# Performance work log

Measured on AMD Instinct MI355X. Metric: run time of the kernel, lower is better.

The kernel has to match this reference:

```python
import jax, jax.numpy as jnp
import numpy as np

NUM_EXPERTS = 8
TOP_K = 2
N_EMBD = 1024
D_FFN = 2048  # 4*N_EMBD // TOP_K, already multiple of BLOCK_N=128
BLOCK_M = 128
NORM_TOPK = True


def setup_inputs() -> dict:
    key = jax.random.key(0)
    k1, k2, k3 = jax.random.split(key, 3)
    x = jax.random.normal(k1, (2, 2048, N_EMBD), dtype=jnp.float32)
    router_w = jax.random.normal(k2, (NUM_EXPERTS, N_EMBD), dtype=jnp.float32) * 0.02
    w1 = jax.random.normal(k3, (N_EMBD, D_FFN * NUM_EXPERTS), dtype=jnp.float32) * 0.02
    return {"x": x, "router_w": router_w, "w1": w1}


def reference(x, router_w, w1):
    B, S, H = x.shape
    x_flat = x.reshape(-1, H)                                   # [T, H]
    router_logits = x_flat @ router_w.T                         # [T, E]
    probs = jax.nn.softmax(router_logits.astype(jnp.float32), axis=-1)
    rweights, sel = jax.lax.top_k(probs, TOP_K)                 # [T, k]
    if NORM_TOPK:
        rweights = rweights / rweights.sum(axis=-1, keepdims=True)
    rweights = rweights.astype(x.dtype)

    # repeat_interleave tokens top_k times, then stable-sort by expert id
    x_rep = jnp.repeat(x_flat, TOP_K, axis=0)                   # [M, H]
    sel_rep = sel.reshape(-1)                                   # [M]
    rw_rep = rweights.reshape(-1, 1)                            # [M, 1]
    order = jnp.argsort(sel_rep, stable=True)                   # expert-sort permutation
    x_grouped = x_rep[order]                                    # [M, H]
    sel_sorted = sel_rep[order]                                 # [M]
    rw_sorted = rw_rep[order]                                   # [M, 1]

    M = x_grouped.shape[0]
    nblk = M // BLOCK_M                                         # M divisible by BLOCK_M by construction
    # SDD kernel: expert of the first row of each BLOCK_M block selects w1 slice
    block_expert = sel_sorted[::BLOCK_M]                        # [nblk] == col_indices_ptr
    w1e = w1.reshape(H, NUM_EXPERTS, D_FFN)                     # w1[:, e*D:(e+1)*D] == w1e[:, e, :]
    w_blk = jnp.take(w1e, block_expert, axis=1)                 # [H, nblk, D]
    x_blk = x_grouped.reshape(nblk, BLOCK_M, H)                 # [nblk, Bm, H]
    block_sparse = jnp.einsum('bmh,hbd->bmd', x_blk, w_blk).reshape(M, D_FFN)

    block_sparse = jax.nn.gelu(block_sparse, approximate=False) * rw_sorted
    return block_sparse, router_logits
```

## Files before the change

### kernel.cpp

```cpp
#include <hip/hip_runtime.h>
#include <hip/hip_bf16.h>
#include <cmath>

typedef float f32x16 __attribute__((ext_vector_type(16)));
typedef __bf16 bf16x8 __attribute__((ext_vector_type(8)));
typedef __bf16 bf16x4 __attribute__((ext_vector_type(4)));

#define NE 8
#define H 1024
#define DF 2048
#define WCOLS 16384
#define NTOK 4096
#define MROWS 8192
#define NBLK 64


typedef const __attribute__((address_space(1))) unsigned int glb_u32;
typedef __attribute__((address_space(3))) unsigned int lds_u32;

__device__ __forceinline__ void async_load16(const void* g, void* l) {
    __builtin_amdgcn_global_load_lds((glb_u32*)g, (lds_u32*)l, 16, 0, 0);
}

__global__ __launch_bounds__(256) void router_kernel(
    const float* __restrict__ x, const float* __restrict__ rw,
    float* __restrict__ logits, int* __restrict__ sel, float* __restrict__ rwn,
    __bf16* __restrict__ xb)
{
    int b = blockIdx.x;
    int tid = threadIdx.x;
    int tok  = b * 4 + (tid >> 6);
    int lane = tid & 63;
    const float* xr = x + (size_t)tok * H;
    __bf16* xbr = xb + (size_t)tok * H;
    float acc[NE];
#pragma unroll
    for (int e = 0; e < NE; ++e) acc[e] = 0.f;
#pragma unroll
    for (int it = 0; it < 4; ++it) {
        int k = (it * 64 + lane) * 4;
        float4 xv = *(const float4*)(xr + k);
        bf16x4 xc;
        xc[0] = (__bf16)xv.x; xc[1] = (__bf16)xv.y;
        xc[2] = (__bf16)xv.z; xc[3] = (__bf16)xv.w;
        *(bf16x4*)(xbr + k) = xc;
#pragma unroll
        for (int e = 0; e < NE; ++e) {
            float4 wv = *(const float4*)(rw + e * H + k);
            acc[e] += xv.x * wv.x + xv.y * wv.y + xv.z * wv.z + xv.w * wv.w;
        }
    }
#pragma unroll
    for (int e = 0; e < NE; ++e) {
        float v = acc[e];
#pragma unroll
        for (int off = 32; off > 0; off >>= 1) v += __shfl_xor(v, off, 64);
        acc[e] = v;
    }
    if (lane == 0) {
#pragma unroll
        for (int e = 0; e < NE; ++e) logits[tok * NE + e] = acc[e];
        int i1 = 0; float m1 = acc[0];
#pragma unroll
        for (int e = 1; e < NE; ++e) if (acc[e] > m1) { m1 = acc[e]; i1 = e; }
        int i2 = -1; float m2 = -INFINITY;
#pragma unroll
        for (int e = 0; e < NE; ++e) if (e != i1 && acc[e] > m2) { m2 = acc[e]; i2 = e; }
        float e2 = expf(m2 - m1);
        float inv = 1.f / (1.f + e2);
        sel[tok * 2]     = i1;  sel[tok * 2 + 1] = i2;
        rwn[tok * 2]     = inv; rwn[tok * 2 + 1] = e2 * inv;
    }
}

__global__ __launch_bounds__(256) void mid_kernel(
    const float* __restrict__ w1, __bf16* __restrict__ Wt,
    const int* __restrict__ sel, const float* __restrict__ rwn,
    int* __restrict__ stok, float* __restrict__ srw, int* __restrict__ bexp)
{
    __shared__ int cnt[NE][256];
    __shared__ int wtot[NE];
    __shared__ int ebase[NE + 1];
    int b = blockIdx.x;
    int t = threadIdx.x;

    if (b < 8192) {
        int q = b * 256 + t;
        int row   = q & 31;
        int chunk = (q >> 5) & 3;
        int grp   = (q >> 7) & 7;
        int kb    = (q >> 10) & 31;
        int ep    = q >> 15;
        int col   = ep * 256 + grp * 32 + row;
        int k0    = kb * 32 + chunk * 8;
        const float* src = w1 + (size_t)k0 * WCOLS + col;
        bf16x8 o;
#pragma unroll
        for (int j = 0; j < 8; ++j) o[j] = (__bf16)src[(size_t)j * WCOLS];
        *(bf16x8*)(Wt + (size_t)q * 8) = o;
        return;
    }

    int selv[32];
    int lc[NE];
#pragma unroll
    for (int e = 0; e < NE; ++e) lc[e] = 0;
    int base = t * 32;
#pragma unroll
    for (int j = 0; j < 32; ++j) { selv[j] = sel[base + j]; lc[selv[j]]++; }
#pragma unroll
    for (int e = 0; e < NE; ++e) cnt[e][t] = lc[e];
    __syncthreads();
    int l = t & 63;
#pragma unroll
    for (int ee = 0; ee < 2; ++ee) {
        int e = (t >> 6) * 2 + ee;
        int s = 0, pre[4];
#pragma unroll
        for (int i = 0; i < 4; ++i) { pre[i] = s; s += cnt[e][l * 4 + i]; }
        int inc = s;
#pragma unroll
        for (int d = 1; d < 64; d <<= 1) {
            int v = __shfl_up(inc, d, 64);
            if (l >= d) inc += v;
        }
        if (l == 63) wtot[e] = inc;
        int excl = inc - s;
#pragma unroll
        for (int i = 0; i < 4; ++i) cnt[e][l * 4 + i] = excl + pre[i];
    }
    __syncthreads();
    if (t == 0) {
        int acc = 0;
        for (int e = 0; e < NE; ++e) { ebase[e] = acc; acc += wtot[e]; }
        ebase[NE] = acc;
    }
    __syncthreads();
    int off[NE];
#pragma unroll
    for (int e = 0; e < NE; ++e) off[e] = ebase[e] + cnt[e][t];
#pragma unroll
    for (int j = 0; j < 32; ++j) {
        int i = base + j;
        int e = selv[j];
        int pos = off[e]++;
        stok[pos] = i >> 1;
        srw[pos]  = rwn[i];
    }
    __syncthreads();
    if (t < NBLK) {
        int r = t * 128;
        int e = 0;
        while (e < NE - 1 && r >= ebase[e + 1]) ++e;
        bexp[t] = e;
    }
}

__global__ __launch_bounds__(256, 4) void moe_gemm(
    const __bf16* __restrict__ xb, const __bf16* __restrict__ Wt,
    const int* __restrict__ stok, const float* __restrict__ srw,
    const int* __restrict__ bexp, float* __restrict__ out)
{
    __shared__ __align__(16) __bf16 smem[3 * 4096];
    __shared__ int   tokS[128];
    __shared__ float rwS[128];

    int g = blockIdx.x;
    int by = (g & 7) * 8 + ((g >> 3) & 7);
    int bx = g >> 6;
    int tid = threadIdx.x;
    if (tid < 128) {
        tokS[tid] = stok[by * 128 + tid];
        rwS[tid]  = srw[by * 128 + tid];
    }
    int e = bexp[by];
    __syncthreads();

    int lane = tid & 63;
    int wv   = tid >> 6;
    int l32  = lane & 31;
    int hi   = lane >> 5;

    const __bf16* aSrcT = xb + (size_t)tokS[(tid >> 6) * 32 + (tid & 31)] * H
                             + ((tid >> 5) & 1) * 8;
    const __bf16* bSrcT = Wt + (size_t)(e * 8 + (bx >> 1)) * 262144
                             + ((bx & 1) * 4 + (tid >> 6)) * 1024
                             + ((tid * 8) & 511);
    __bf16* aDst = smem + tid * 8;
    __bf16* bDst = smem + 2048 + tid * 8;

#define STAGE(kt_, bb_) do {                                                   \
        int koff_ = (((kt_) >> 1) << 13) + (((kt_) & 1) << 9);                 \
        async_load16(aSrcT + (kt_) * 16, aDst + (bb_) * 4096);                 \
        async_load16(bSrcT + koff_,      bDst + (bb_) * 4096);                 \
    } while (0)

    int wm = (wv & 1) * 64;
    int wn = (wv >> 1) * 64;
    int agb = (wv & 1) * 2;
    int bgb = (wv >> 1) * 2;
    int rdo = hi * 256 + l32 * 8;

    f32x16 acc[2][2];
#pragma unroll
    for (int i = 0; i < 2; ++i)
#pragma unroll
        for (int j = 0; j < 2; ++j)
#pragma unroll
            for (int r = 0; r < 16; ++r) acc[i][j][r] = 0.f;

    STAGE(0, 0);
    STAGE(1, 1);

    int cur = 0;
    for (int kt = 0; kt < 64; ++kt) {
        if (kt < 63) asm volatile("s_waitcnt vmcnt(2)" ::: "memory");
        else         asm volatile("s_waitcnt vmcnt(0)" ::: "memory");
        __builtin_amdgcn_s_barrier();
        __builtin_amdgcn_sched_barrier(0);
        int nb = cur + 2; if (nb >= 3) nb -= 3;
        if (kt < 62) STAGE(kt + 2, nb);

        const __bf16* Ab = smem + cur * 4096;
        bf16x8 af[2], bfr[2];
#pragma unroll
        for (int ti = 0; ti < 2; ++ti)
            af[ti]  = *(const bf16x8*)&Ab[(agb + ti) * 512 + rdo];
#pragma unroll
        for (int tj = 0; tj < 2; ++tj)
            bfr[tj] = *(const bf16x8*)&Ab[2048 + (bgb + tj) * 512 + rdo];

        __builtin_amdgcn_s_setprio(1);
#pragma unroll
        for (int ti = 0; ti < 2; ++ti)
#pragma unroll
            for (int tj = 0; tj < 2; ++tj)
                acc[ti][tj] = __builtin_amdgcn_mfma_f32_32x32x16_bf16(
                    af[ti], bfr[tj], acc[ti][tj], 0, 0, 0);
        __builtin_amdgcn_s_setprio(0);

        cur = cur + 1; if (cur >= 3) cur -= 3;
    }
#undef STAGE

    int rowh = hi * 4;
#pragma unroll
    for (int ti = 0; ti < 2; ++ti)
#pragma unroll
        for (int reg = 0; reg < 16; ++reg) {
            int row = (reg & 3) + 8 * (reg >> 2) + rowh;
            int m = wm + ti * 32 + row;
            float rw = rwS[m];
            size_t ob = (size_t)(by * 128 + m) * DF + bx * 128 + wn + l32;
#pragma unroll
            for (int tj = 0; tj < 2; ++tj) {
                float val = acc[ti][tj][reg];
                float u = 0.7978845608028654f * val * (1.f + 0.044715f * val * val);
                float t = __expf(-2.f * fabsf(u));
                float th = (1.f - t) / (1.f + t);
                th = u < 0.f ? -th : th;
                out[ob + tj * 32] = 0.5f * val * (1.f + th) * rw;
            }
        }
}

extern "C" void kernel_launch(void* const* d_in, const int* in_sizes, int n_in,
                              void* d_out, int out_size, void* d_ws, size_t ws_size,
                              hipStream_t stream) {
    (void)in_sizes; (void)n_in; (void)out_size; (void)ws_size;
    const float* x        = (const float*)d_in[0];
    const float* router_w = (const float*)d_in[1];
    const float* w1       = (const float*)d_in[2];
    float* out    = (float*)d_out;
    float* logits = out + (size_t)MROWS * DF;

    char* ws    = (char*)d_ws;
    int*   sel  = (int*)(ws);
    float* rwn  = (float*)(ws + 0x8000);
    int*   stok = (int*)(ws + 0x10000);
    float* srw  = (float*)(ws + 0x18000);
    int*   bexp = (int*)(ws + 0x20000);
    __bf16* xb  = (__bf16*)(ws + (1 << 20));
    __bf16* Wt  = (__bf16*)(ws + (1 << 20) + (8 << 20));

    router_kernel<<<1024, 256, 0, stream>>>(x, router_w, logits, sel, rwn, xb);
    mid_kernel<<<8193, 256, 0, stream>>>(w1, Wt, sel, rwn, stok, srw, bexp);
    moe_gemm<<<1024, 256, 0, stream>>>(xb, Wt, stok, srw, bexp, out);
}
```

Measured before the change: 200.8 us.

## Coalesce w1 bf16 transpose via LDS tile and load B fragments directly to registers

The weight conversion kernel now reads w1 with coalesced float4 loads into a shared-memory tile and transposes there before writing bf16 fragments. The old version did strided per-column global reads. The GEMM no longer stages B through LDS. Each wave loads its B fragments straight from global memory into registers, one k-step ahead, while A keeps a 4-deep async LDS ring. This cuts LDS traffic and removes the strided w1 reads, but B loads become per-wave global reads that other waves cannot share, and the vmcnt accounting must stay correct.

```diff
diff --git a/kernel.cpp b/kernel.cpp
--- a/kernel.cpp
+++ b/kernel.cpp
@@ -78,26 +78,38 @@
     const int* __restrict__ sel, const float* __restrict__ rwn,
     int* __restrict__ stok, float* __restrict__ srw, int* __restrict__ bexp)
 {
+    __shared__ float tile[32][132];
     __shared__ int cnt[NE][256];
     __shared__ int wtot[NE];
     __shared__ int ebase[NE + 1];
     int b = blockIdx.x;
     int t = threadIdx.x;
 
-    if (b < 8192) {
-        int q = b * 256 + t;
-        int row   = q & 31;
-        int chunk = (q >> 5) & 3;
-        int grp   = (q >> 7) & 7;
-        int kb    = (q >> 10) & 31;
-        int ep    = q >> 15;
-        int col   = ep * 256 + grp * 32 + row;
-        int k0    = kb * 32 + chunk * 8;
-        const float* src = w1 + (size_t)k0 * WCOLS + col;
-        bf16x8 o;
-#pragma unroll
-        for (int j = 0; j < 8; ++j) o[j] = (__bf16)src[(size_t)j * WCOLS];
-        *(bf16x8*)(Wt + (size_t)q * 8) = o;
+    if (b < 4096) {
+        int c  = b >> 5;
+        int kb = b & 31;
+        int kk = t >> 3;
+        int cc = (t & 7) * 16;
+        const float* src = w1 + (size_t)(kb * 32 + kk) * WCOLS + c * 128 + cc;
+#pragma unroll
+        for (int i = 0; i < 4; ++i) {
+            float4 v = *(const float4*)(src + i * 4);
+            *(float4*)&tile[kk][cc + i * 4] = v;
+        }
+        __syncthreads();
+        int n = t >> 1, kc0 = (t & 1) * 16;
+        bf16x8 o0, o1;
+#pragma unroll
+        for (int i = 0; i < 8; ++i) {
+            o0[i] = (__bf16)tile[kc0 + i][n];
+            o1[i] = (__bf16)tile[kc0 + 8 + i][n];
+        }
+        size_t tile_id = (size_t)(c >> 1) * 32 + kb;
+        int group  = (c & 1) * 4 + (n >> 5);
+        int chunk0 = kc0 >> 3;
+        __bf16* dst = Wt + tile_id * 8192 + group * 1024 + chunk0 * 256 + (n & 31) * 8;
+        *(bf16x8*)dst         = o0;
+        *(bf16x8*)(dst + 256) = o1;
         return;
     }
 
@@ -161,7 +173,7 @@
     const int* __restrict__ stok, const float* __restrict__ srw,
     const int* __restrict__ bexp, float* __restrict__ out)
 {
-    __shared__ __align__(16) __bf16 smem[3 * 4096];
+    __shared__ __align__(16) __bf16 smem[4 * 2048];
     __shared__ int   tokS[128];
     __shared__ float rwS[128];
 
@@ -183,22 +195,22 @@
 
     const __bf16* aSrcT = xb + (size_t)tokS[(tid >> 6) * 32 + (tid & 31)] * H
                              + ((tid >> 5) & 1) * 8;
-    const __bf16* bSrcT = Wt + (size_t)(e * 8 + (bx >> 1)) * 262144
-                             + ((bx & 1) * 4 + (tid >> 6)) * 1024
-                             + ((tid * 8) & 511);
-    __bf16* aDst = smem + tid * 8;
-    __bf16* bDst = smem + 2048 + tid * 8;
-
-#define STAGE(kt_, bb_) do {                                                   \
-        int koff_ = (((kt_) >> 1) << 13) + (((kt_) & 1) << 9);                 \
-        async_load16(aSrcT + (kt_) * 16, aDst + (bb_) * 4096);                 \
-        async_load16(bSrcT + koff_,      bDst + (bb_) * 4096);                 \
+    __bf16* aDstT = smem + tid * 8;
+    const __bf16* bBase = Wt + (size_t)(e * 8 + (bx >> 1)) * 262144
+                             + (size_t)((bx & 1) * 4 + (wv >> 1) * 2) * 1024
+                             + hi * 256 + l32 * 8;
+
+#define STAGE_A(kt_) async_load16(aSrcT + (kt_) * 16, aDstT + ((kt_) & 3) * 2048)
+#define LOAD_B(dst_, kt_)                                                      \
+    do {                                                                       \
+        const __bf16* p_ = bBase + ((kt_) >> 1) * 8192 + ((kt_) & 1) * 512;    \
+        dst_[0] = *(const bf16x8*)(p_);                                        \
+        dst_[1] = *(const bf16x8*)(p_ + 1024);                                 \
     } while (0)
 
-    int wm = (wv & 1) * 64;
-    int wn = (wv >> 1) * 64;
+    int wm  = (wv & 1) * 64;
+    int wn  = (wv >> 1) * 64;
     int agb = (wv & 1) * 2;
-    int bgb = (wv >> 1) * 2;
     int rdo = hi * 256 + l32 * 8;
 
     f32x16 acc[2][2];
@@ -209,39 +221,48 @@
 #pragma unroll
             for (int r = 0; r < 16; ++r) acc[i][j][r] = 0.f;
 
-    STAGE(0, 0);
-    STAGE(1, 1);
-
-    int cur = 0;
-    for (int kt = 0; kt < 64; ++kt) {
-        if (kt < 63) asm volatile("s_waitcnt vmcnt(2)" ::: "memory");
-        else         asm volatile("s_waitcnt vmcnt(0)" ::: "memory");
+    bf16x8 bE[2], bO[2];
+
+    STAGE_A(0);
+    STAGE_A(1);
+    LOAD_B(bE, 0);
+
+    for (int kt = 0; kt < 64; kt += 2) {
+        asm volatile("s_waitcnt vmcnt(3)" ::: "memory");
         __builtin_amdgcn_s_barrier();
         __builtin_amdgcn_sched_barrier(0);
-        int nb = cur + 2; if (nb >= 3) nb -= 3;
-        if (kt < 62) STAGE(kt + 2, nb);
-
-        const __bf16* Ab = smem + cur * 4096;
-        bf16x8 af[2], bfr[2];
-#pragma unroll
-        for (int ti = 0; ti < 2; ++ti)
-            af[ti]  = *(const bf16x8*)&Ab[(agb + ti) * 512 + rdo];
-#pragma unroll
-        for (int tj = 0; tj < 2; ++tj)
-            bfr[tj] = *(const bf16x8*)&Ab[2048 + (bgb + tj) * 512 + rdo];
-
-        __builtin_amdgcn_s_setprio(1);
-#pragma unroll
-        for (int ti = 0; ti < 2; ++ti)
-#pragma unroll
-            for (int tj = 0; tj < 2; ++tj)
-                acc[ti][tj] = __builtin_amdgcn_mfma_f32_32x32x16_bf16(
-                    af[ti], bfr[tj], acc[ti][tj], 0, 0, 0);
-        __builtin_amdgcn_s_setprio(0);
-
-        cur = cur + 1; if (cur >= 3) cur -= 3;
-    }
-#undef STAGE
+        if (kt + 2 < 64) STAGE_A(kt + 2);
+        LOAD_B(bO, kt + 1);
+        {
+            const __bf16* Ab = smem + (kt & 3) * 2048;
+            bf16x8 af0 = *(const bf16x8*)&Ab[(agb + 0) * 512 + rdo];
+            bf16x8 af1 = *(const bf16x8*)&Ab[(agb + 1) * 512 + rdo];
+            __builtin_amdgcn_s_setprio(1);
+            acc[0][0] = __builtin_amdgcn_mfma_f32_32x32x16_bf16(af0, bE[0], acc[0][0], 0, 0, 0);
+            acc[0][1] = __builtin_amdgcn_mfma_f32_32x32x16_bf16(af0, bE[1], acc[0][1], 0, 0, 0);
+            acc[1][0] = __builtin_amdgcn_mfma_f32_32x32x16_bf16(af1, bE[0], acc[1][0], 0, 0, 0);
+            acc[1][1] = __builtin_amdgcn_mfma_f32_32x32x16_bf16(af1, bE[1], acc[1][1], 0, 0, 0);
+            __builtin_amdgcn_s_setprio(0);
+        }
+        asm volatile("s_waitcnt vmcnt(3)" ::: "memory");
+        __builtin_amdgcn_s_barrier();
+        __builtin_amdgcn_sched_barrier(0);
+        if (kt + 3 < 64) STAGE_A(kt + 3);
+        if (kt + 2 < 64) LOAD_B(bE, kt + 2);
+        {
+            const __bf16* Ab = smem + ((kt + 1) & 3) * 2048;
+            bf16x8 af0 = *(const bf16x8*)&Ab[(agb + 0) * 512 + rdo];
+            bf16x8 af1 = *(const bf16x8*)&Ab[(agb + 1) * 512 + rdo];
+            __builtin_amdgcn_s_setprio(1);
+            acc[0][0] = __builtin_amdgcn_mfma_f32_32x32x16_bf16(af0, bO[0], acc[0][0], 0, 0, 0);
+            acc[0][1] = __builtin_amdgcn_mfma_f32_32x32x16_bf16(af0, bO[1], acc[0][1], 0, 0, 0);
+            acc[1][0] = __builtin_amdgcn_mfma_f32_32x32x16_bf16(af1, bO[0], acc[1][0], 0, 0, 0);
+            acc[1][1] = __builtin_amdgcn_mfma_f32_32x32x16_bf16(af1, bO[1], acc[1][1], 0, 0, 0);
+            __builtin_amdgcn_s_setprio(0);
+        }
+    }
+#undef STAGE_A
+#undef LOAD_B
 
     int rowh = hi * 4;
 #pragma unroll
@@ -284,6 +305,6 @@
     __bf16* Wt  = (__bf16*)(ws + (1 << 20) + (8 << 20));
 
     router_kernel<<<1024, 256, 0, stream>>>(x, router_w, logits, sel, rwn, xb);
-    mid_kernel<<<8193, 256, 0, stream>>>(w1, Wt, sel, rwn, stok, srw, bexp);
+    mid_kernel<<<4097, 256, 0, stream>>>(w1, Wt, sel, rwn, stok, srw, bexp);
     moe_gemm<<<1024, 256, 0, stream>>>(xb, Wt, stok, srw, bexp, out);
 }
```

New measurement: 204.8 us. 2.0% more time.

## Coalesce w1 transpose via LDS tile, merge with router, deepen GEMM K-step

Applied to the files above, without the earlier changes.

The w1 fp32-to-bf16 repack now stages a 32x128 tile through LDS and reads it with coalesced float4 loads, replacing the old per-thread column-strided scalar reads. That repack is merged into the router kernel's launch, and the token sort moves to its own single-block kernel. The GEMM K-step doubles to 32 (two MFMAs per fragment pair per stage), which halves barrier count but doubles LDS per stage and lowers occupancy to 3 waves per SIMD.

```diff
diff --git a/kernel.cpp b/kernel.cpp
--- a/kernel.cpp
+++ b/kernel.cpp
@@ -22,85 +22,95 @@
     __builtin_amdgcn_global_load_lds((glb_u32*)g, (lds_u32*)l, 16, 0, 0);
 }
 
-__global__ __launch_bounds__(256) void router_kernel(
+__global__ __launch_bounds__(256) void prep_kernel(
     const float* __restrict__ x, const float* __restrict__ rw,
+    const float* __restrict__ w1,
     float* __restrict__ logits, int* __restrict__ sel, float* __restrict__ rwn,
-    __bf16* __restrict__ xb)
+    __bf16* __restrict__ xb, __bf16* __restrict__ Wt)
 {
+    __shared__ float tile[32][132];
     int b = blockIdx.x;
     int tid = threadIdx.x;
-    int tok  = b * 4 + (tid >> 6);
-    int lane = tid & 63;
-    const float* xr = x + (size_t)tok * H;
-    __bf16* xbr = xb + (size_t)tok * H;
-    float acc[NE];
-#pragma unroll
-    for (int e = 0; e < NE; ++e) acc[e] = 0.f;
-#pragma unroll
-    for (int it = 0; it < 4; ++it) {
-        int k = (it * 64 + lane) * 4;
-        float4 xv = *(const float4*)(xr + k);
-        bf16x4 xc;
-        xc[0] = (__bf16)xv.x; xc[1] = (__bf16)xv.y;
-        xc[2] = (__bf16)xv.z; xc[3] = (__bf16)xv.w;
-        *(bf16x4*)(xbr + k) = xc;
+    if (b < 1024) {
+        int tok  = b * 4 + (tid >> 6);
+        int lane = tid & 63;
+        const float* xr = x + (size_t)tok * H;
+        __bf16* xbr = xb + (size_t)tok * H;
+        float acc[NE];
+#pragma unroll
+        for (int e = 0; e < NE; ++e) acc[e] = 0.f;
+#pragma unroll
+        for (int it = 0; it < 4; ++it) {
+            int k = (it * 64 + lane) * 4;
+            float4 xv = *(const float4*)(xr + k);
+            bf16x4 xc;
+            xc[0] = (__bf16)xv.x; xc[1] = (__bf16)xv.y;
+            xc[2] = (__bf16)xv.z; xc[3] = (__bf16)xv.w;
+            *(bf16x4*)(xbr + k) = xc;
+#pragma unroll
+            for (int e = 0; e < NE; ++e) {
+                float4 wv = *(const float4*)(rw + e * H + k);
+                acc[e] += xv.x * wv.x + xv.y * wv.y + xv.z * wv.z + xv.w * wv.w;
+            }
+        }
 #pragma unroll
         for (int e = 0; e < NE; ++e) {
-            float4 wv = *(const float4*)(rw + e * H + k);
-            acc[e] += xv.x * wv.x + xv.y * wv.y + xv.z * wv.z + xv.w * wv.w;
-        }
-    }
-#pragma unroll
-    for (int e = 0; e < NE; ++e) {
-        float v = acc[e];
-#pragma unroll
-        for (int off = 32; off > 0; off >>= 1) v += __shfl_xor(v, off, 64);
-        acc[e] = v;
-    }
-    if (lane == 0) {
-#pragma unroll
-        for (int e = 0; e < NE; ++e) logits[tok * NE + e] = acc[e];
-        int i1 = 0; float m1 = acc[0];
-#pragma unroll
-        for (int e = 1; e < NE; ++e) if (acc[e] > m1) { m1 = acc[e]; i1 = e; }
-        int i2 = -1; float m2 = -INFINITY;
-#pragma unroll
-        for (int e = 0; e < NE; ++e) if (e != i1 && acc[e] > m2) { m2 = acc[e]; i2 = e; }
-        float e2 = expf(m2 - m1);
-        float inv = 1.f / (1.f + e2);
-        sel[tok * 2]     = i1;  sel[tok * 2 + 1] = i2;
-        rwn[tok * 2]     = inv; rwn[tok * 2 + 1] = e2 * inv;
-    }
-}
-
-__global__ __launch_bounds__(256) void mid_kernel(
-    const float* __restrict__ w1, __bf16* __restrict__ Wt,
+            float v = acc[e];
+#pragma unroll
+            for (int off = 32; off > 0; off >>= 1) v += __shfl_xor(v, off, 64);
+            acc[e] = v;
+        }
+        if (lane == 0) {
+#pragma unroll
+            for (int e = 0; e < NE; ++e) logits[tok * NE + e] = acc[e];
+            int i1 = 0; float m1 = acc[0];
+#pragma unroll
+            for (int e = 1; e < NE; ++e) if (acc[e] > m1) { m1 = acc[e]; i1 = e; }
+            int i2 = -1; float m2 = -INFINITY;
+#pragma unroll
+            for (int e = 0; e < NE; ++e) if (e != i1 && acc[e] > m2) { m2 = acc[e]; i2 = e; }
+            float e2 = expf(m2 - m1);
+            float inv = 1.f / (1.f + e2);
+            sel[tok * 2]     = i1;  sel[tok * 2 + 1] = i2;
+            rwn[tok * 2]     = inv; rwn[tok * 2 + 1] = e2 * inv;
+        }
+        return;
+    }
+    int g  = b - 1024;
+    int c  = g >> 5;
+    int kb = g & 31;
+    int kk = tid >> 3;
+    int cc = (tid & 7) * 16;
+    const float* src = w1 + (size_t)(kb * 32 + kk) * WCOLS + c * 128 + cc;
+#pragma unroll
+    for (int i = 0; i < 4; ++i) {
+        float4 v = *(const float4*)(src + i * 4);
+        *(float4*)&tile[kk][cc + i * 4] = v;
+    }
+    __syncthreads();
+    int n = tid >> 1, kc0 = (tid & 1) * 16;
+    bf16x8 o0, o1;
+#pragma unroll
+    for (int i = 0; i < 8; ++i) {
+        o0[i] = (__bf16)tile[kc0 + i][n];
+        o1[i] = (__bf16)tile[kc0 + 8 + i][n];
+    }
+    size_t tile_id = (size_t)(c >> 1) * 32 + kb;
+    int group  = (c & 1) * 4 + (n >> 5);
+    int chunk0 = kc0 >> 3;
+    __bf16* dst = Wt + tile_id * 8192 + group * 1024 + chunk0 * 256 + (n & 31) * 8;
+    *(bf16x8*)dst         = o0;
+    *(bf16x8*)(dst + 256) = o1;
+}
+
+__global__ __launch_bounds__(256) void sort_kernel(
     const int* __restrict__ sel, const float* __restrict__ rwn,
     int* __restrict__ stok, float* __restrict__ srw, int* __restrict__ bexp)
 {
     __shared__ int cnt[NE][256];
     __shared__ int wtot[NE];
     __shared__ int ebase[NE + 1];
-    int b = blockIdx.x;
     int t = threadIdx.x;
-
-    if (b < 8192) {
-        int q = b * 256 + t;
-        int row   = q & 31;
-        int chunk = (q >> 5) & 3;
-        int grp   = (q >> 7) & 7;
-        int kb    = (q >> 10) & 31;
-        int ep    = q >> 15;
-        int col   = ep * 256 + grp * 32 + row;
-        int k0    = kb * 32 + chunk * 8;
-        const float* src = w1 + (size_t)k0 * WCOLS + col;
-        bf16x8 o;
-#pragma unroll
-        for (int j = 0; j < 8; ++j) o[j] = (__bf16)src[(size_t)j * WCOLS];
-        *(bf16x8*)(Wt + (size_t)q * 8) = o;
-        return;
-    }
-
     int selv[32];
     int lc[NE];
 #pragma unroll
@@ -156,12 +166,12 @@
     }
 }
 
-__global__ __launch_bounds__(256, 4) void moe_gemm(
+__global__ __launch_bounds__(256, 3) void moe_gemm(
     const __bf16* __restrict__ xb, const __bf16* __restrict__ Wt,
     const int* __restrict__ stok, const float* __restrict__ srw,
     const int* __restrict__ bexp, float* __restrict__ out)
 {
-    __shared__ __align__(16) __bf16 smem[3 * 4096];
+    __shared__ __align__(16) __bf16 smem[3 * 8192];
     __shared__ int   tokS[128];
     __shared__ float rwS[128];
 
@@ -181,22 +191,26 @@
     int l32  = lane & 31;
     int hi   = lane >> 5;
 
-    const __bf16* aSrcT = xb + (size_t)tokS[(tid >> 6) * 32 + (tid & 31)] * H
-                             + ((tid >> 5) & 1) * 8;
+    int c0 = (tid >> 5) & 1;
+    const __bf16* aSrcT = xb + (size_t)tokS[(tid >> 6) * 32 + (tid & 31)] * H + c0 * 8;
+    __bf16* aDstT = smem + (tid >> 6) * 1024 + c0 * 256 + (tid & 31) * 8;
     const __bf16* bSrcT = Wt + (size_t)(e * 8 + (bx >> 1)) * 262144
-                             + ((bx & 1) * 4 + (tid >> 6)) * 1024
-                             + ((tid * 8) & 511);
-    __bf16* aDst = smem + tid * 8;
-    __bf16* bDst = smem + 2048 + tid * 8;
+                             + (bx & 1) * 4096 + tid * 8;
+    __bf16* bDstT = smem + 4096 + tid * 8;
 
 #define STAGE(kt_, bb_) do {                                                   \
-        int koff_ = (((kt_) >> 1) << 13) + (((kt_) & 1) << 9);                 \
-        async_load16(aSrcT + (kt_) * 16, aDst + (bb_) * 4096);                 \
-        async_load16(bSrcT + koff_,      bDst + (bb_) * 4096);                 \
+        const __bf16* a_ = aSrcT + (kt_) * 32;                                 \
+        __bf16* ad_ = aDstT + (bb_) * 8192;                                    \
+        async_load16(a_,      ad_);                                            \
+        async_load16(a_ + 16, ad_ + 512);                                      \
+        const __bf16* b_ = bSrcT + (size_t)(kt_) * 8192;                       \
+        __bf16* bd_ = bDstT + (bb_) * 8192;                                    \
+        async_load16(b_,        bd_);                                          \
+        async_load16(b_ + 2048, bd_ + 2048);                                   \
     } while (0)
 
-    int wm = (wv & 1) * 64;
-    int wn = (wv >> 1) * 64;
+    int wm  = (wv & 1) * 64;
+    int wn  = (wv >> 1) * 64;
     int agb = (wv & 1) * 2;
     int bgb = (wv >> 1) * 2;
     int rdo = hi * 256 + l32 * 8;
@@ -213,30 +227,35 @@
     STAGE(1, 1);
 
     int cur = 0;
-    for (int kt = 0; kt < 64; ++kt) {
-        if (kt < 63) asm volatile("s_waitcnt vmcnt(2)" ::: "memory");
+    for (int kt = 0; kt < 32; ++kt) {
+        if (kt < 31) asm volatile("s_waitcnt vmcnt(4)" ::: "memory");
         else         asm volatile("s_waitcnt vmcnt(0)" ::: "memory");
         __builtin_amdgcn_s_barrier();
         __builtin_amdgcn_sched_barrier(0);
         int nb = cur + 2; if (nb >= 3) nb -= 3;
-        if (kt < 62) STAGE(kt + 2, nb);
-
-        const __bf16* Ab = smem + cur * 4096;
-        bf16x8 af[2], bfr[2];
-#pragma unroll
-        for (int ti = 0; ti < 2; ++ti)
-            af[ti]  = *(const bf16x8*)&Ab[(agb + ti) * 512 + rdo];
-#pragma unroll
-        for (int tj = 0; tj < 2; ++tj)
-            bfr[tj] = *(const bf16x8*)&Ab[2048 + (bgb + tj) * 512 + rdo];
-
+        if (kt < 30) STAGE(kt + 2, nb);
+
+        const __bf16* Ab = smem + cur * 8192;
+        bf16x8 af[2][2], bfr[2][2];
+#pragma unroll
+        for (int h = 0; h < 2; ++h) {
+            int co = h * 512 + rdo;
+#pragma unroll
+            for (int ti = 0; ti < 2; ++ti)
+                af[ti][h]  = *(const bf16x8*)&Ab[(agb + ti) * 1024 + co];
+#pragma unroll
+            for (int tj = 0; tj < 2; ++tj)
+                bfr[tj][h] = *(const bf16x8*)&Ab[4096 + (bgb + tj) * 1024 + co];
+        }
         __builtin_amdgcn_s_setprio(1);
 #pragma unroll
-        for (int ti = 0; ti < 2; ++ti)
-#pragma unroll
-            for (int tj = 0; tj < 2; ++tj)
-                acc[ti][tj] = __builtin_amdgcn_mfma_f32_32x32x16_bf16(
-                    af[ti], bfr[tj], acc[ti][tj], 0, 0, 0);
+        for (int h = 0; h < 2; ++h)
+#pragma unroll
+            for (int ti = 0; ti < 2; ++ti)
+#pragma unroll
+                for (int tj = 0; tj < 2; ++tj)
+                    acc[ti][tj] = __builtin_amdgcn_mfma_f32_32x32x16_bf16(
+                        af[ti][h], bfr[tj][h], acc[ti][tj], 0, 0, 0);
         __builtin_amdgcn_s_setprio(0);
 
         cur = cur + 1; if (cur >= 3) cur -= 3;
@@ -283,7 +302,7 @@
     __bf16* xb  = (__bf16*)(ws + (1 << 20));
     __bf16* Wt  = (__bf16*)(ws + (1 << 20) + (8 << 20));
 
-    router_kernel<<<1024, 256, 0, stream>>>(x, router_w, logits, sel, rwn, xb);
-    mid_kernel<<<8193, 256, 0, stream>>>(w1, Wt, sel, rwn, stok, srw, bexp);
+    prep_kernel<<<5120, 256, 0, stream>>>(x, router_w, w1, logits, sel, rwn, xb, Wt);
+    sort_kernel<<<1, 256, 0, stream>>>(sel, rwn, stok, srw, bexp);
     moe_gemm<<<1024, 256, 0, stream>>>(xb, Wt, stok, srw, bexp, out);
 }
```

New measurement: 209.9 us. +4.5%, slower.
